# Kernel optimization log

Measured on AMD Instinct MI355X. Metric: run time of the kernel, lower is better.

## Reference

```python
import jax, jax.numpy as jnp
import numpy as np

EPS = 1e-5  # torch LayerNorm default


def _layer_norm(x, gamma, beta):
    mu = jnp.mean(x, axis=-1, keepdims=True)
    var = jnp.mean(jnp.square(x - mu), axis=-1, keepdims=True)
    return (x - mu) * jax.lax.rsqrt(var + EPS) * gamma + beta


def setup_inputs() -> dict:
    key = jax.random.key(0)
    ks = jax.random.split(key, 6)
    B, T, S, A, H = 256, 2048, 39, 4, 256
    D = S + A
    observations = jax.random.normal(ks[0], (B, T, S), dtype=jnp.float32)
    actions = jax.random.normal(ks[1], (B, T, A), dtype=jnp.float32)
    # MLP params (orthogonal gain=0.1 in torch; random scale 0.1 here)
    W1 = jax.random.normal(ks[2], (D, H), dtype=jnp.float32) * 0.1
    b1 = jnp.zeros((H,), dtype=jnp.float32)
    g1 = jnp.ones((H,), dtype=jnp.float32)
    beta1 = jnp.zeros((H,), dtype=jnp.float32)
    W2 = jax.random.normal(ks[3], (H, H), dtype=jnp.float32) * 0.1
    b2 = jnp.zeros((H,), dtype=jnp.float32)
    g2 = jnp.ones((H,), dtype=jnp.float32)
    beta2 = jnp.zeros((H,), dtype=jnp.float32)
    W3 = jax.random.normal(ks[4], (H, 1), dtype=jnp.float32) * 0.1
    b3 = jnp.zeros((1,), dtype=jnp.float32)
    return {"observations": observations, "actions": actions,
            "W1": W1, "b1": b1, "g1": g1, "beta1": beta1,
            "W2": W2, "b2": b2, "g2": g2, "beta2": beta2,
            "W3": W3, "b3": b3}


def reference(observations, actions, W1, b1, g1, beta1, W2, b2, g2, beta2, W3, b3):
    # Batched equivalent of the per-(b,t) loop: concat -> (Linear+LN+ReLU) x2 -> Linear(.,1)
    x = jnp.concatenate([observations, actions], axis=-1)  # [B, T, S+A]
    h = jax.nn.relu(_layer_norm(x @ W1 + b1, g1, beta1))    # [B, T, H]
    h = jax.nn.relu(_layer_norm(h @ W2 + b2, g2, beta2))    # [B, T, H]
    r = (h @ W3 + b3)[..., 0]                                # [B, T] per-step reward
    return jnp.sum(r, axis=-1)                               # [B] segment reward
```

## Files before the change

### kernel.cpp

```cpp
#include <hip/hip_runtime.h>
#include <hip/hip_bf16.h>

typedef __attribute__((ext_vector_type(8))) short short8;
typedef __attribute__((ext_vector_type(4))) float f32x4;

#define NT 2048
#define ROWS_PER_BLOCK 128
#define NROWS_WAVE 32

__device__ __forceinline__ short f2bf(float x) {
  __hip_bfloat16 h = __float2bfloat16(x);
  return __builtin_bit_cast(short, h);
}

__global__ void zero_out_kernel(float* __restrict__ out, int n) {
  int i = blockIdx.x * blockDim.x + threadIdx.x;
  if (i < n) out[i] = 0.f;
}

__global__ void repack_kernel(const float* __restrict__ W1, const float* __restrict__ W2,
                              short* __restrict__ Wp) {
  int id = blockIdx.x * 256 + threadIdx.x;
  const float* W; int kmax; long dstbase; int f;
  if (id < 2048) { f = id;        W = W1; kmax = 43;  dstbase = (long)f * 8; }
  else           { f = id - 2048; W = W2; kmax = 256; dstbase = 2048L * 8 + (long)f * 8; }
  int lane = f & 63; int ts = f >> 6; int t = ts & 15; int s = ts >> 4;
  int k0 = s * 32 + (lane >> 4) * 8;
  int n  = t * 16 + (lane & 15);
  short8 v;
  #pragma unroll
  for (int i = 0; i < 8; ++i) {
    int k = k0 + i;
    float x = (k < kmax) ? W[(long)k * 256 + n] : 0.f;
    v[i] = f2bf(x);
  }
  *(short8*)(Wp + dstbase) = v;
}

__launch_bounds__(256, 2)
__global__ void srm_mfma(const float* __restrict__ obs, const float* __restrict__ act,
                         const float* __restrict__ b1, const float* __restrict__ g1,
                         const float* __restrict__ be1,
                         const float* __restrict__ b2, const float* __restrict__ g2,
                         const float* __restrict__ be2,
                         const float* __restrict__ W3, const float* __restrict__ b3,
                         const short* __restrict__ Wp, float* __restrict__ out) {
  __shared__ float  bl1[16][20], bl2[16][20], w3l[16][20];
  __shared__ float2 gbl1[16][18], gbl2[16][18];
  __shared__ short  H1buf[4][NROWS_WAVE * 256];

  const int tid = threadIdx.x;
  const int wave = tid >> 6, lane = tid & 63;
  const int lr = lane & 15, lg = lane >> 4;

  {
    int c = tid;
    bl1[c & 15][c >> 4] = b1[c];
    bl2[c & 15][c >> 4] = b2[c];
    w3l[c & 15][c >> 4] = W3[c];
    gbl1[c & 15][c >> 4] = make_float2(g1[c], be1[c]);
    gbl2[c & 15][c >> 4] = make_float2(g2[c], be2[c]);
  }
  __syncthreads();

  const int row0 = blockIdx.x * ROWS_PER_BLOCK + wave * NROWS_WAVE;
  const int bidx = row0 / NT;
  const float b3v = b3[0];

  short* H1 = &H1buf[wave][0];
  const short8* W1v = (const short8*)Wp;
  const short8* W2v = (const short8*)(Wp + 2048L * 8);

  f32x4 acc[2][16];
  #pragma unroll
  for (int rt = 0; rt < 2; ++rt)
    #pragma unroll
    for (int t = 0; t < 16; ++t) acc[rt][t] = (f32x4)0.f;

  #pragma unroll
  for (int s = 0; s < 2; ++s) {
    short8 a[2];
    #pragma unroll
    for (int rt = 0; rt < 2; ++rt) {
      const int row = row0 + rt * 16 + lr;
      #pragma unroll
      for (int i = 0; i < 8; ++i) {
        int k = s * 32 + lg * 8 + i;
        float x = 0.f;
        if (k < 39)      x = obs[(long)row * 39 + k];
        else if (k < 43) x = act[(long)row * 4 + (k - 39)];
        a[rt][i] = f2bf(x);
      }
    }
    #pragma unroll
    for (int t = 0; t < 16; ++t) {
      short8 bf = W1v[(s * 16 + t) * 64 + lane];
      acc[0][t] = __builtin_amdgcn_mfma_f32_16x16x32_bf16(a[0], bf, acc[0][t], 0, 0, 0);
      acc[1][t] = __builtin_amdgcn_mfma_f32_16x16x32_bf16(a[1], bf, acc[1][t], 0, 0, 0);
    }
  }

  f32x4 mean_[2], rstd_[2];

  {
    f32x4 s_[2] = {(f32x4)0.f, (f32x4)0.f}, q_[2] = {(f32x4)0.f, (f32x4)0.f};
    #pragma unroll
    for (int t0 = 0; t0 < 4; ++t0) {
      f32x4 bv = *(const f32x4*)&bl1[lr][t0 * 4];
      #pragma unroll
      for (int j = 0; j < 4; ++j) {
        int t = t0 * 4 + j;
        #pragma unroll
        for (int rt = 0; rt < 2; ++rt) {
          f32x4 v = acc[rt][t] + bv[j];
          acc[rt][t] = v;
          s_[rt] += v; q_[rt] += v * v;
        }
      }
    }
    #pragma unroll
    for (int rt = 0; rt < 2; ++rt)
      #pragma unroll
      for (int qd = 0; qd < 4; ++qd) {
        float s = s_[rt][qd], q = q_[rt][qd];
        #pragma unroll
        for (int off = 1; off < 16; off <<= 1) { s += __shfl_xor(s, off); q += __shfl_xor(q, off); }
        float m = s * (1.f / 256.f);
        float var = q * (1.f / 256.f) - m * m;
        mean_[rt][qd] = m;
        rstd_[rt][qd] = rsqrtf(var + 1e-5f);
      }
  }

  #pragma unroll
  for (int t2 = 0; t2 < 8; ++t2) {
    f32x4 gg = *(const f32x4*)&gbl1[lr][t2 * 2];
    #pragma unroll
    for (int hh = 0; hh < 2; ++hh) {
      int t = t2 * 2 + hh;
      float g_ = gg[hh * 2], be_ = gg[hh * 2 + 1];
      int colb = t * 16 + lr;
      #pragma unroll
      for (int rt = 0; rt < 2; ++rt) {
        f32x4 v = (acc[rt][t] - mean_[rt]) * rstd_[rt] * g_ + be_;
        #pragma unroll
        for (int qd = 0; qd < 4; ++qd) {
          float vv = fmaxf(v[qd], 0.f);
          int row = rt * 16 + lg * 4 + qd;
          H1[row * 256 + (colb ^ ((row & 7) << 3))] = f2bf(vv);
        }
      }
    }
  }

  #pragma unroll
  for (int rt = 0; rt < 2; ++rt)
    #pragma unroll
    for (int t = 0; t < 16; ++t) acc[rt][t] = (f32x4)0.f;

  #pragma unroll 2
  for (int s = 0; s < 8; ++s) {
    short8 a[2];
    #pragma unroll
    for (int rt = 0; rt < 2; ++rt) {
      int arow = rt * 16 + lr;
      a[rt] = *(const short8*)&H1[arow * 256 + ((s * 32 + lg * 8) ^ ((arow & 7) << 3))];
    }
    #pragma unroll
    for (int t = 0; t < 16; ++t) {
      short8 bf = W2v[(s * 16 + t) * 64 + lane];
      acc[0][t] = __builtin_amdgcn_mfma_f32_16x16x32_bf16(a[0], bf, acc[0][t], 0, 0, 0);
      acc[1][t] = __builtin_amdgcn_mfma_f32_16x16x32_bf16(a[1], bf, acc[1][t], 0, 0, 0);
    }
  }

  {
    f32x4 s_[2] = {(f32x4)0.f, (f32x4)0.f}, q_[2] = {(f32x4)0.f, (f32x4)0.f};
    #pragma unroll
    for (int t0 = 0; t0 < 4; ++t0) {
      f32x4 bv = *(const f32x4*)&bl2[lr][t0 * 4];
      #pragma unroll
      for (int j = 0; j < 4; ++j) {
        int t = t0 * 4 + j;
        #pragma unroll
        for (int rt = 0; rt < 2; ++rt) {
          f32x4 v = acc[rt][t] + bv[j];
          acc[rt][t] = v;
          s_[rt] += v; q_[rt] += v * v;
        }
      }
    }
    #pragma unroll
    for (int rt = 0; rt < 2; ++rt)
      #pragma unroll
      for (int qd = 0; qd < 4; ++qd) {
        float s = s_[rt][qd], q = q_[rt][qd];
        #pragma unroll
        for (int off = 1; off < 16; off <<= 1) { s += __shfl_xor(s, off); q += __shfl_xor(q, off); }
        float m = s * (1.f / 256.f);
        float var = q * (1.f / 256.f) - m * m;
        mean_[rt][qd] = m;
        rstd_[rt][qd] = rsqrtf(var + 1e-5f);
      }
  }

  float p = 0.f;
  #pragma unroll
  for (int t0 = 0; t0 < 4; ++t0) {
    f32x4 wv = *(const f32x4*)&w3l[lr][t0 * 4];
    #pragma unroll
    for (int h2 = 0; h2 < 2; ++h2) {
      f32x4 gg = *(const f32x4*)&gbl2[lr][t0 * 4 + h2 * 2];
      #pragma unroll
      for (int hh = 0; hh < 2; ++hh) {
        int t = t0 * 4 + h2 * 2 + hh;
        float g_ = gg[hh * 2], be_ = gg[hh * 2 + 1];
        float w_ = wv[h2 * 2 + hh];
        #pragma unroll
        for (int rt = 0; rt < 2; ++rt) {
          f32x4 v = (acc[rt][t] - mean_[rt]) * rstd_[rt] * g_ + be_;
          #pragma unroll
          for (int qd = 0; qd < 4; ++qd) p += fmaxf(v[qd], 0.f) * w_;
        }
      }
    }
  }
  #pragma unroll
  for (int off = 1; off < 64; off <<= 1) p += __shfl_xor(p, off);
  if (lane == 0) atomicAdd(&out[bidx], p + 32.f * b3v);
}

extern "C" void kernel_launch(void* const* d_in, const int* in_sizes, int n_in,
                              void* d_out, int out_size, void* d_ws, size_t ws_size,
                              hipStream_t stream) {
  const float* obs = (const float*)d_in[0];
  const float* act = (const float*)d_in[1];
  const float* W1  = (const float*)d_in[2];
  const float* b1  = (const float*)d_in[3];
  const float* g1  = (const float*)d_in[4];
  const float* be1 = (const float*)d_in[5];
  const float* W2  = (const float*)d_in[6];
  const float* b2  = (const float*)d_in[7];
  const float* g2  = (const float*)d_in[8];
  const float* be2 = (const float*)d_in[9];
  const float* W3  = (const float*)d_in[10];
  const float* b3  = (const float*)d_in[11];
  float* out = (float*)d_out;

  zero_out_kernel<<<1, 256, 0, stream>>>(out, out_size);

  short* Wp = (short*)d_ws;
  repack_kernel<<<40, 256, 0, stream>>>(W1, W2, Wp);

  const int n_rows = 256 * 2048;
  srm_mfma<<<n_rows / ROWS_PER_BLOCK, 256, 0, stream>>>(
      obs, act, b1, g1, be1, b2, g2, be2, W3, b3, Wp, out);
}
```

Baseline: 334.1 us.

## Switch to transposed 32x32x16 MFMA with register-resident hidden activations

Measured after the change: 376.2 us. 12.6% more time.

```diff
diff --git a/kernel.cpp b/kernel.cpp
--- a/kernel.cpp
+++ b/kernel.cpp
@@ -1,232 +1,207 @@
 #include <hip/hip_runtime.h>
 #include <hip/hip_bf16.h>
 
-typedef __attribute__((ext_vector_type(8))) short short8;
-typedef __attribute__((ext_vector_type(4))) float f32x4;
-
-#define NT 2048
-#define ROWS_PER_BLOCK 128
-#define NROWS_WAVE 32
-
-__device__ __forceinline__ short f2bf(float x) {
+typedef __attribute__((ext_vector_type(8)))  short short8;
+typedef __attribute__((ext_vector_type(4)))  float f32x4;
+typedef __attribute__((ext_vector_type(16))) float f32x16;
+
+__device__ __forceinline__ unsigned short f2bf(float x) {
   __hip_bfloat16 h = __float2bfloat16(x);
-  return __builtin_bit_cast(short, h);
-}
-
-__global__ void zero_out_kernel(float* __restrict__ out, int n) {
-  int i = blockIdx.x * blockDim.x + threadIdx.x;
-  if (i < n) out[i] = 0.f;
-}
-
-__global__ void repack_kernel(const float* __restrict__ W1, const float* __restrict__ W2,
-                              short* __restrict__ Wp) {
+  return (unsigned short)__builtin_bit_cast(short, h);
+}
+__device__ __forceinline__ unsigned packbf2(float lo, float hi2) {
+  return (unsigned)f2bf(lo) | ((unsigned)f2bf(hi2) << 16);
+}
+
+__global__ void repack_zero(const float* __restrict__ W1, const float* __restrict__ W2,
+                            short* __restrict__ Wp, float* __restrict__ out, int outn) {
   int id = blockIdx.x * 256 + threadIdx.x;
-  const float* W; int kmax; long dstbase; int f;
-  if (id < 2048) { f = id;        W = W1; kmax = 43;  dstbase = (long)f * 8; }
-  else           { f = id - 2048; W = W2; kmax = 256; dstbase = 2048L * 8 + (long)f * 8; }
-  int lane = f & 63; int ts = f >> 6; int t = ts & 15; int s = ts >> 4;
-  int k0 = s * 32 + (lane >> 4) * 8;
-  int n  = t * 16 + (lane & 15);
+  if (blockIdx.x == 0 && threadIdx.x < outn) out[threadIdx.x] = 0.f;
+  if (id >= 152 * 64) return;
+  int fragidx = id >> 6, lane = id & 63;
+  const float* W; int ks, mt, kmax;
+  if (fragidx < 24) { W = W1; ks = fragidx >> 3; mt = fragidx & 7; kmax = 43; }
+  else { int f2 = fragidx - 24; W = W2; ks = f2 >> 3; mt = f2 & 7; kmax = 256; }
+  int h = 32 * mt + (lane & 31);
+  int k0 = 16 * ks + 8 * (lane >> 5);
   short8 v;
   #pragma unroll
   for (int i = 0; i < 8; ++i) {
     int k = k0 + i;
-    float x = (k < kmax) ? W[(long)k * 256 + n] : 0.f;
-    v[i] = f2bf(x);
-  }
-  *(short8*)(Wp + dstbase) = v;
+    float x = (k < kmax) ? W[(long)k * 256 + h] : 0.f;
+    v[i] = (short)f2bf(x);
+  }
+  *(short8*)(Wp + (long)fragidx * 512 + lane * 8) = v;
+}
+
+__device__ __forceinline__ short8 pack8(const float* v) {
+  union { unsigned u[4]; short8 s; } c;
+  #pragma unroll
+  for (int j = 0; j < 4; ++j) c.u[j] = packbf2(v[2 * j], v[2 * j + 1]);
+  return c.s;
 }
 
 __launch_bounds__(256, 2)
-__global__ void srm_mfma(const float* __restrict__ obs, const float* __restrict__ act,
-                         const float* __restrict__ b1, const float* __restrict__ g1,
-                         const float* __restrict__ be1,
-                         const float* __restrict__ b2, const float* __restrict__ g2,
-                         const float* __restrict__ be2,
-                         const float* __restrict__ W3, const float* __restrict__ b3,
-                         const short* __restrict__ Wp, float* __restrict__ out) {
-  __shared__ float  bl1[16][20], bl2[16][20], w3l[16][20];
-  __shared__ float2 gbl1[16][18], gbl2[16][18];
-  __shared__ short  H1buf[4][NROWS_WAVE * 256];
-
+__global__ void srm2(const float* __restrict__ obs, const float* __restrict__ act,
+                     const float* __restrict__ b1, const float* __restrict__ g1,
+                     const float* __restrict__ be1,
+                     const float* __restrict__ b2, const float* __restrict__ g2,
+                     const float* __restrict__ be2,
+                     const float* __restrict__ W3, const float* __restrict__ b3,
+                     const short* __restrict__ Wp, float* __restrict__ out) {
+  __shared__ float pb1[256], pg1[256], pe1[256];
+  __shared__ float pb2[256], pg2[256], pe2[256], pw3[256];
   const int tid = threadIdx.x;
+  pb1[tid] = b1[tid]; pg1[tid] = g1[tid]; pe1[tid] = be1[tid];
+  pb2[tid] = b2[tid]; pg2[tid] = g2[tid]; pe2[tid] = be2[tid];
+  pw3[tid] = W3[tid];
+  const float b3v = b3[0];
+  __syncthreads();
+
   const int wave = tid >> 6, lane = tid & 63;
-  const int lr = lane & 15, lg = lane >> 4;
-
+  const int l31 = lane & 31, hi = lane >> 5;
+  const int row0 = blockIdx.x * 128 + wave * 32;
+  const int n = row0 + l31;
+  const int bidx = row0 >> 11;
+
+  const float* orow = obs + (long)n * 39;
+  const float* arow = act + (long)n * 4;
+  short8 bx0, bx1, bx2;
   {
-    int c = tid;
-    bl1[c & 15][c >> 4] = b1[c];
-    bl2[c & 15][c >> 4] = b2[c];
-    w3l[c & 15][c >> 4] = W3[c];
-    gbl1[c & 15][c >> 4] = make_float2(g1[c], be1[c]);
-    gbl2[c & 15][c >> 4] = make_float2(g2[c], be2[c]);
-  }
-  __syncthreads();
-
-  const int row0 = blockIdx.x * ROWS_PER_BLOCK + wave * NROWS_WAVE;
-  const int bidx = row0 / NT;
-  const float b3v = b3[0];
-
-  short* H1 = &H1buf[wave][0];
+    float v[8];
+    #pragma unroll
+    for (int i = 0; i < 8; ++i) v[i] = orow[8 * hi + i];
+    bx0 = pack8(v);
+    #pragma unroll
+    for (int i = 0; i < 8; ++i) v[i] = orow[16 + 8 * hi + i];
+    bx1 = pack8(v);
+    #pragma unroll
+    for (int i = 0; i < 8; ++i) {
+      int k = 32 + 8 * hi + i;
+      float t = 0.f;
+      if (k < 39) t = orow[k]; else if (k < 43) t = arow[k - 39];
+      v[i] = t;
+    }
+    bx2 = pack8(v);
+  }
+
   const short8* W1v = (const short8*)Wp;
-  const short8* W2v = (const short8*)(Wp + 2048L * 8);
-
-  f32x4 acc[2][16];
-  #pragma unroll
-  for (int rt = 0; rt < 2; ++rt)
-    #pragma unroll
-    for (int t = 0; t < 16; ++t) acc[rt][t] = (f32x4)0.f;
-
-  #pragma unroll
-  for (int s = 0; s < 2; ++s) {
-    short8 a[2];
-    #pragma unroll
-    for (int rt = 0; rt < 2; ++rt) {
-      const int row = row0 + rt * 16 + lr;
-      #pragma unroll
-      for (int i = 0; i < 8; ++i) {
-        int k = s * 32 + lg * 8 + i;
-        float x = 0.f;
-        if (k < 39)      x = obs[(long)row * 39 + k];
-        else if (k < 43) x = act[(long)row * 4 + (k - 39)];
-        a[rt][i] = f2bf(x);
-      }
-    }
-    #pragma unroll
-    for (int t = 0; t < 16; ++t) {
-      short8 bf = W1v[(s * 16 + t) * 64 + lane];
-      acc[0][t] = __builtin_amdgcn_mfma_f32_16x16x32_bf16(a[0], bf, acc[0][t], 0, 0, 0);
-      acc[1][t] = __builtin_amdgcn_mfma_f32_16x16x32_bf16(a[1], bf, acc[1][t], 0, 0, 0);
-    }
-  }
-
-  f32x4 mean_[2], rstd_[2];
-
+  const short8* W2v = (const short8*)(Wp + 24L * 512);
+
+  f32x16 acc[8];
+  #pragma unroll
+  for (int mt = 0; mt < 8; ++mt) acc[mt] = (f32x16)0.f;
+
+  #pragma unroll
+  for (int ks = 0; ks < 3; ++ks) {
+    const short8 bb = (ks == 0) ? bx0 : (ks == 1) ? bx1 : bx2;
+    #pragma unroll
+    for (int mt = 0; mt < 8; ++mt) {
+      short8 a = W1v[(ks * 8 + mt) * 64 + lane];
+      acc[mt] = __builtin_amdgcn_mfma_f32_32x32x16_bf16(a, bb, acc[mt], 0, 0, 0);
+    }
+  }
+
+  float mean1, rstd1;
   {
-    f32x4 s_[2] = {(f32x4)0.f, (f32x4)0.f}, q_[2] = {(f32x4)0.f, (f32x4)0.f};
-    #pragma unroll
-    for (int t0 = 0; t0 < 4; ++t0) {
-      f32x4 bv = *(const f32x4*)&bl1[lr][t0 * 4];
-      #pragma unroll
-      for (int j = 0; j < 4; ++j) {
-        int t = t0 * 4 + j;
+    float s = 0.f, q = 0.f;
+    #pragma unroll
+    for (int mt = 0; mt < 8; ++mt)
+      #pragma unroll
+      for (int qq = 0; qq < 4; ++qq) {
+        const f32x4 b4 = *(const f32x4*)&pb1[32 * mt + 8 * qq + 4 * hi];
         #pragma unroll
-        for (int rt = 0; rt < 2; ++rt) {
-          f32x4 v = acc[rt][t] + bv[j];
-          acc[rt][t] = v;
-          s_[rt] += v; q_[rt] += v * v;
+        for (int e = 0; e < 4; ++e) {
+          float t = acc[mt][4 * qq + e] + b4[e];
+          acc[mt][4 * qq + e] = t;
+          s += t; q += t * t;
         }
       }
-    }
-    #pragma unroll
-    for (int rt = 0; rt < 2; ++rt)
-      #pragma unroll
-      for (int qd = 0; qd < 4; ++qd) {
-        float s = s_[rt][qd], q = q_[rt][qd];
+    s += __shfl_xor(s, 32); q += __shfl_xor(q, 32);
+    mean1 = s * (1.f / 256.f);
+    rstd1 = rsqrtf(q * (1.f / 256.f) - mean1 * mean1 + 1e-5f);
+  }
+
+  unsigned pk[8][4][2];
+  #pragma unroll
+  for (int mt = 0; mt < 8; ++mt)
+    #pragma unroll
+    for (int qq = 0; qq < 4; ++qq) {
+      const int h0 = 32 * mt + 8 * qq + 4 * hi;
+      const f32x4 g4 = *(const f32x4*)&pg1[h0];
+      const f32x4 e4 = *(const f32x4*)&pe1[h0];
+      float val[4];
+      #pragma unroll
+      for (int e = 0; e < 4; ++e) {
+        float a = rstd1 * g4[e];
+        float c = e4[e] - mean1 * a;
+        val[e] = fmaxf(acc[mt][4 * qq + e] * a + c, 0.f);
+      }
+      pk[mt][qq][0] = packbf2(val[0], val[1]);
+      pk[mt][qq][1] = packbf2(val[2], val[3]);
+    }
+
+  #pragma unroll
+  for (int mt = 0; mt < 8; ++mt) acc[mt] = (f32x16)0.f;
+
+  #pragma unroll
+  for (int ks = 0; ks < 16; ++ks) {
+    const int msrc = ks >> 1, q0 = 2 * (ks & 1), q1 = q0 + 1;
+    unsigned c0 = hi ? pk[msrc][q0][0] : pk[msrc][q1][0];
+    unsigned c1 = hi ? pk[msrc][q0][1] : pk[msrc][q1][1];
+    unsigned r0 = __shfl_xor(c0, 32), r1 = __shfl_xor(c1, 32);
+    unsigned o0 = hi ? pk[msrc][q1][0] : pk[msrc][q0][0];
+    unsigned o1 = hi ? pk[msrc][q1][1] : pk[msrc][q0][1];
+    union { unsigned u[4]; short8 s; } bb;
+    bb.u[0] = hi ? r0 : o0; bb.u[1] = hi ? r1 : o1;
+    bb.u[2] = hi ? o0 : r0; bb.u[3] = hi ? o1 : r1;
+    #pragma unroll
+    for (int mt = 0; mt < 8; ++mt) {
+      short8 a = W2v[(ks * 8 + mt) * 64 + lane];
+      acc[mt] = __builtin_amdgcn_mfma_f32_32x32x16_bf16(a, bb.s, acc[mt], 0, 0, 0);
+    }
+  }
+
+  float mean2, rstd2;
+  {
+    float s = 0.f, q = 0.f;
+    #pragma unroll
+    for (int mt = 0; mt < 8; ++mt)
+      #pragma unroll
+      for (int qq = 0; qq < 4; ++qq) {
+        const f32x4 b4 = *(const f32x4*)&pb2[32 * mt + 8 * qq + 4 * hi];
         #pragma unroll
-        for (int off = 1; off < 16; off <<= 1) { s += __shfl_xor(s, off); q += __shfl_xor(q, off); }
-        float m = s * (1.f / 256.f);
-        float var = q * (1.f / 256.f) - m * m;
-        mean_[rt][qd] = m;
-        rstd_[rt][qd] = rsqrtf(var + 1e-5f);
-      }
-  }
-
-  #pragma unroll
-  for (int t2 = 0; t2 < 8; ++t2) {
-    f32x4 gg = *(const f32x4*)&gbl1[lr][t2 * 2];
-    #pragma unroll
-    for (int hh = 0; hh < 2; ++hh) {
-      int t = t2 * 2 + hh;
-      float g_ = gg[hh * 2], be_ = gg[hh * 2 + 1];
-      int colb = t * 16 + lr;
-      #pragma unroll
-      for (int rt = 0; rt < 2; ++rt) {
-        f32x4 v = (acc[rt][t] - mean_[rt]) * rstd_[rt] * g_ + be_;
-        #pragma unroll
-        for (int qd = 0; qd < 4; ++qd) {
-          float vv = fmaxf(v[qd], 0.f);
-          int row = rt * 16 + lg * 4 + qd;
-          H1[row * 256 + (colb ^ ((row & 7) << 3))] = f2bf(vv);
+        for (int e = 0; e < 4; ++e) {
+          float t = acc[mt][4 * qq + e] + b4[e];
+          acc[mt][4 * qq + e] = t;
+          s += t; q += t * t;
         }
       }
-    }
-  }
-
-  #pragma unroll
-  for (int rt = 0; rt < 2; ++rt)
-    #pragma unroll
-    for (int t = 0; t < 16; ++t) acc[rt][t] = (f32x4)0.f;
-
-  #pragma unroll 2
-  for (int s = 0; s < 8; ++s) {
-    short8 a[2];
-    #pragma unroll
-    for (int rt = 0; rt < 2; ++rt) {
-      int arow = rt * 16 + lr;
-      a[rt] = *(const short8*)&H1[arow * 256 + ((s * 32 + lg * 8) ^ ((arow & 7) << 3))];
-    }
-    #pragma unroll
-    for (int t = 0; t < 16; ++t) {
-      short8 bf = W2v[(s * 16 + t) * 64 + lane];
-      acc[0][t] = __builtin_amdgcn_mfma_f32_16x16x32_bf16(a[0], bf, acc[0][t], 0, 0, 0);
-      acc[1][t] = __builtin_amdgcn_mfma_f32_16x16x32_bf16(a[1], bf, acc[1][t], 0, 0, 0);
-    }
-  }
-
-  {
-    f32x4 s_[2] = {(f32x4)0.f, (f32x4)0.f}, q_[2] = {(f32x4)0.f, (f32x4)0.f};
-    #pragma unroll
-    for (int t0 = 0; t0 < 4; ++t0) {
-      f32x4 bv = *(const f32x4*)&bl2[lr][t0 * 4];
-      #pragma unroll
-      for (int j = 0; j < 4; ++j) {
-        int t = t0 * 4 + j;
-        #pragma unroll
-        for (int rt = 0; rt < 2; ++rt) {
-          f32x4 v = acc[rt][t] + bv[j];
-          acc[rt][t] = v;
-          s_[rt] += v; q_[rt] += v * v;
-        }
-      }
-    }
-    #pragma unroll
-    for (int rt = 0; rt < 2; ++rt)
-      #pragma unroll
-      for (int qd = 0; qd < 4; ++qd) {
-        float s = s_[rt][qd], q = q_[rt][qd];
-        #pragma unroll
-        for (int off = 1; off < 16; off <<= 1) { s += __shfl_xor(s, off); q += __shfl_xor(q, off); }
-        float m = s * (1.f / 256.f);
-        float var = q * (1.f / 256.f) - m * m;
-        mean_[rt][qd] = m;
-        rstd_[rt][qd] = rsqrtf(var + 1e-5f);
-      }
+    s += __shfl_xor(s, 32); q += __shfl_xor(q, 32);
+    mean2 = s * (1.f / 256.f);
+    rstd2 = rsqrtf(q * (1.f / 256.f) - mean2 * mean2 + 1e-5f);
   }
 
   float p = 0.f;
   #pragma unroll
-  for (int t0 = 0; t0 < 4; ++t0) {
-    f32x4 wv = *(const f32x4*)&w3l[lr][t0 * 4];
-    #pragma unroll
-    for (int h2 = 0; h2 < 2; ++h2) {
-      f32x4 gg = *(const f32x4*)&gbl2[lr][t0 * 4 + h2 * 2];
-      #pragma unroll
-      for (int hh = 0; hh < 2; ++hh) {
-        int t = t0 * 4 + h2 * 2 + hh;
-        float g_ = gg[hh * 2], be_ = gg[hh * 2 + 1];
-        float w_ = wv[h2 * 2 + hh];
-        #pragma unroll
-        for (int rt = 0; rt < 2; ++rt) {
-          f32x4 v = (acc[rt][t] - mean_[rt]) * rstd_[rt] * g_ + be_;
-          #pragma unroll
-          for (int qd = 0; qd < 4; ++qd) p += fmaxf(v[qd], 0.f) * w_;
-        }
-      }
-    }
-  }
-  #pragma unroll
-  for (int off = 1; off < 64; off <<= 1) p += __shfl_xor(p, off);
+  for (int mt = 0; mt < 8; ++mt)
+    #pragma unroll
+    for (int qq = 0; qq < 4; ++qq) {
+      const int h0 = 32 * mt + 8 * qq + 4 * hi;
+      const f32x4 g4 = *(const f32x4*)&pg2[h0];
+      const f32x4 e4 = *(const f32x4*)&pe2[h0];
+      const f32x4 w4 = *(const f32x4*)&pw3[h0];
+      #pragma unroll
+      for (int e = 0; e < 4; ++e) {
+        float a = rstd2 * g4[e];
+        float c = e4[e] - mean2 * a;
+        float val = fmaxf(acc[mt][4 * qq + e] * a + c, 0.f);
+        p += val * w4[e];
+      }
+    }
+  p += __shfl_xor(p, 32);
+  #pragma unroll
+  for (int off = 1; off < 32; off <<= 1) p += __shfl_xor(p, off);
   if (lane == 0) atomicAdd(&out[bidx], p + 32.f * b3v);
 }
 
@@ -247,12 +222,11 @@
   const float* b3  = (const float*)d_in[11];
   float* out = (float*)d_out;
 
-  zero_out_kernel<<<1, 256, 0, stream>>>(out, out_size);
-
   short* Wp = (short*)d_ws;
-  repack_kernel<<<40, 256, 0, stream>>>(W1, W2, Wp);
+
+  repack_zero<<<38, 256, 0, stream>>>(W1, W2, Wp, out, out_size);
 
   const int n_rows = 256 * 2048;
-  srm_mfma<<<n_rows / ROWS_PER_BLOCK, 256, 0, stream>>>(
-      obs, act, b1, g1, be1, b2, g2, be2, W3, b3, Wp, out);
-}
+  srm2<<<n_rows / 128, 256, 0, stream>>>(obs, act, b1, g1, be1,
+                                         b2, g2, be2, W3, b3, Wp, out);
+}
```
